# Kernel tuning notes

Hardware: AMD Instinct MI355X
Metric: run time of the kernel (lower is better)

Reference implementation:

```python
import jax, jax.numpy as jnp
import numpy as np

EMBED_DIM = 1024
NUM_HEADS = 16
HEAD_DIM = EMBED_DIM // NUM_HEADS


def setup_inputs() -> dict:
    key = jax.random.key(0)
    ks = jax.random.split(key, 9)
    B, S, D = 2, 2048, EMBED_DIM
    scale = 1.0 / np.sqrt(D)
    x = jax.random.normal(ks[0], (B, S, D), dtype=jnp.float32)
    # nn.Linear weights are stored as (out, in); y = x @ W.T + b
    Wq = jax.random.uniform(ks[1], (D, D), jnp.float32, -scale, scale)
    bq = jax.random.uniform(ks[2], (D,), jnp.float32, -scale, scale)
    Wk = jax.random.uniform(ks[3], (D, D), jnp.float32, -scale, scale)
    bk = jax.random.uniform(ks[4], (D,), jnp.float32, -scale, scale)
    Wv = jax.random.uniform(ks[5], (D, D), jnp.float32, -scale, scale)
    bv = jax.random.uniform(ks[6], (D,), jnp.float32, -scale, scale)
    Wo = jax.random.uniform(ks[7], (D, D), jnp.float32, -scale, scale)
    bo = jax.random.uniform(ks[8], (D,), jnp.float32, -scale, scale)
    return {"x": x, "Wq": Wq, "bq": bq, "Wk": Wk, "bk": bk,
            "Wv": Wv, "bv": bv, "Wo": Wo, "bo": bo}


def reference(x, Wq, bq, Wk, bk, Wv, bv, Wo, bo):
    B, S, D = x.shape
    H, Hd = NUM_HEADS, HEAD_DIM

    def split_heads(t):  # [B,S,D] -> [B,H,S,Hd]
        return t.reshape(B, S, H, Hd).transpose(0, 2, 1, 3)

    Q = split_heads(x @ Wq.T + bq)
    K = split_heads(x @ Wk.T + bk)
    V = split_heads(x @ Wv.T + bv)

    scores = jnp.einsum('bhqd,bhkd->bhqk', Q, K) / jnp.sqrt(
        jnp.asarray(Hd, dtype=x.dtype))
    attn = jax.nn.softmax(scores, axis=-1)
    out = jnp.einsum('bhqk,bhkd->bhqd', attn, V)  # [B,H,S,Hd]
    out = out.transpose(0, 2, 1, 3).reshape(B, S, D)
    return out @ Wo.T + bo
```

## Files before the change

### kernel.cpp

```cpp
#include <hip/hip_runtime.h>
#include <hip/hip_bf16.h>
#include <stdint.h>

typedef __attribute__((ext_vector_type(8))) short short8;
typedef __attribute__((ext_vector_type(4))) float f32x4;
typedef unsigned short u16;
typedef unsigned int u32;

static constexpr int S = 2048;
static constexpr int H = 16;
static constexpr int HD = 64;

__device__ __forceinline__ float fast_exp2(float x){
  return __builtin_amdgcn_exp2f(x);
}

__device__ __forceinline__ u16 f2bf(float f){
  union { float f; u32 u; } x; x.f = f;
  u32 r = x.u + 0x7fffu + ((x.u >> 16) & 1u);
  return (u16)(r >> 16);
}

__device__ __forceinline__ u32 cvt_pk_bf16(float lo, float hi){
  u32 r;
  asm("v_cvt_pk_bf16_f32 %0, %1, %2" : "=v"(r) : "v"(lo), "v"(hi));
  return r;
}

__global__ __launch_bounds__(256) void cast_all(const float* __restrict__ x,
                                                const float* __restrict__ Wq,
                                                const float* __restrict__ Wk,
                                                const float* __restrict__ Wv,
                                                const float* __restrict__ Wo,
                                                u16* __restrict__ xb,
                                                u16* __restrict__ Wb){
  int i = (blockIdx.x * 256 + threadIdx.x) * 4;
  const float* s; u16* d; int off;
  if (i < 4194304){
    s = x; d = xb; off = i;
  } else {
    int j = i - 4194304;
    int w = j >> 20;
    s = (w == 0) ? Wq : (w == 1) ? Wk : (w == 2) ? Wv : Wo;
    d = Wb + (w << 20);
    off = j & 1048575;
  }
  float4 v = *(const float4*)(s + off);
  ushort4 o;
  o.x = f2bf(v.x); o.y = f2bf(v.y); o.z = f2bf(v.z); o.w = f2bf(v.w);
  *(ushort4*)(d + off) = o;
}

__device__ __forceinline__ void gload_lds16(const void* g, void* lds_uniform){
  __builtin_amdgcn_global_load_lds(
      (const __attribute__((address_space(1))) u32*)g,
      (__attribute__((address_space(3))) u32*)lds_uniform,
      16, 0, 0);
}

__global__ __launch_bounds__(256) void gemm_qkv(const u16* __restrict__ A,
                                                const u16* __restrict__ Wall,
                                                const float* __restrict__ b0p,
                                                const float* __restrict__ b1p,
                                                const float* __restrict__ b2p,
                                                u16* __restrict__ obf){
  __shared__ __align__(16) u16 As[2*128*32];
  __shared__ __align__(16) u16 Bs[2*128*32];

  const int tid  = threadIdx.x;
  const int lane = tid & 63;
  const int wid  = tid >> 6;
  const int wm = wid >> 1, wn = wid & 1;
  const int l4 = lane >> 4, l15 = lane & 15;

  const int L = blockIdx.x + 8*blockIdx.y + 256*blockIdx.z;
  const int W = (L & 7)*96 + (L >> 3);
  const int z = W >> 8;
  const int rem = W & 255;
  const int n0 = (rem & 7) * 128;
  const int m0 = (rem >> 3) * 128;

  const u16* Bw = Wall + (size_t)z * (1024*1024);
  const float* bias = (z == 0) ? b0p : ((z == 1) ? b1p : b2p);

  f32x4 acc[4][4];
  #pragma unroll
  for (int m=0;m<4;m++)
    #pragma unroll
    for (int n=0;n<4;n++) acc[m][n] = (f32x4){0.f,0.f,0.f,0.f};

  const char* Ab = (const char*)A  + (size_t)m0 * 2048;
  const char* Bb = (const char*)Bw + (size_t)n0 * 2048;
  char* AsB = (char*)As;
  char* BsB = (char*)Bs;

  int ldsu[2], row_[2], col_[2];
  #pragma unroll
  for (int p=0;p<2;p++){
    ldsu[p] = wid*1024 + p*4096;
    int b = ldsu[p] + lane*16;
    row_[p] = b >> 6;
    col_[p] = b & 63;
  }

  #pragma unroll
  for (int p=0;p<2;p++){
    gload_lds16(Ab + (size_t)row_[p]*2048 + col_[p], AsB + ldsu[p]);
    gload_lds16(Bb + (size_t)row_[p]*2048 + col_[p], BsB + ldsu[p]);
  }
  __syncthreads();

  for (int kt = 0; kt < 32; ++kt){
    const int cur = kt & 1;
    if (kt + 1 < 32){
      const int nxt = cur ^ 1;
      const int kb = (kt + 1) * 64;
      #pragma unroll
      for (int p=0;p<2;p++){
        gload_lds16(Ab + (size_t)row_[p]*2048 + kb + col_[p], AsB + nxt*8192 + ldsu[p]);
        gload_lds16(Bb + (size_t)row_[p]*2048 + kb + col_[p], BsB + nxt*8192 + ldsu[p]);
      }
    }
    const u16* Asc = (const u16*)(AsB + cur*8192);
    const u16* Bsc = (const u16*)(BsB + cur*8192);

    short8 af[4], bfr[4];
    const int kcol = 8 * l4;
    #pragma unroll
    for (int m=0;m<4;m++)
      af[m] = *(const short8*)&Asc[(wm*64 + m*16 + l15)*32 + kcol];
    #pragma unroll
    for (int n=0;n<4;n++)
      bfr[n] = *(const short8*)&Bsc[(wn*64 + n*16 + l15)*32 + kcol];

    __builtin_amdgcn_s_setprio(1);
    #pragma unroll
    for (int m=0;m<4;m++)
      #pragma unroll
      for (int n=0;n<4;n++)
        acc[m][n] = __builtin_amdgcn_mfma_f32_16x16x32_bf16(af[m], bfr[n], acc[m][n], 0,0,0);
    __builtin_amdgcn_s_setprio(0);

    __syncthreads();
  }

  #pragma unroll
  for (int m=0;m<4;m++){
    const int rgb = m0 + wm*64 + m*16 + 4*l4;
    #pragma unroll
    for (int n=0;n<4;n++){
      const int cg = n0 + wn*64 + n*16 + l15;
      const float bb = bias[cg];
      const int bi = rgb >> 11, si = rgb & 2047;
      const int hi = cg >> 6,  hd = cg & 63;
      if (z == 2){
        u16* outz = obf + (size_t)2 * 4194304u;
        ushort4 o;
        o.x = f2bf(acc[m][n][0] + bb);
        o.y = f2bf(acc[m][n][1] + bb);
        o.z = f2bf(acc[m][n][2] + bb);
        o.w = f2bf(acc[m][n][3] + bb);
        *(ushort4*)&outz[(((size_t)(bi*16 + hi))*64 + hd)*2048 + si] = o;
      } else {
        u16* outz = obf + (size_t)z * 4194304u;
        const float sc = (z == 0) ? 0.18033688011112042f : 1.0f;
        #pragma unroll
        for (int r=0;r<4;r++)
          outz[(((size_t)(bi*16 + hi))*2048 + (si + r))*64 + hd] =
              f2bf((acc[m][n][r] + bb) * sc);
      }
    }
  }
}

__global__ __launch_bounds__(256) void gemm_out(const u16* __restrict__ A,
                                                const u16* __restrict__ Wo,
                                                const float* __restrict__ bo,
                                                float* __restrict__ ofp){
  __shared__ __align__(16) u16 As[2*64*32];
  __shared__ __align__(16) u16 Bs[2*128*32];

  const int tid  = threadIdx.x;
  const int lane = tid & 63;
  const int wid  = tid >> 6;
  const int wm = wid >> 1, wn = wid & 1;
  const int l4 = lane >> 4, l15 = lane & 15;

  const int L = blockIdx.x + 8*blockIdx.y;
  const int W = (L & 7)*64 + (L >> 3);
  const int n0 = (W & 7) * 128;
  const int m0 = (W >> 3) * 64;

  f32x4 acc[2][4];
  #pragma unroll
  for (int m=0;m<2;m++)
    #pragma unroll
    for (int n=0;n<4;n++) acc[m][n] = (f32x4){0.f,0.f,0.f,0.f};

  const char* Ab = (const char*)A  + (size_t)m0 * 2048;
  const char* Bb = (const char*)Wo + (size_t)n0 * 2048;
  char* AsB = (char*)As;
  char* BsB = (char*)Bs;

  const int ldsuA = wid*1024;
  int rowA, colA;
  { int b = ldsuA + lane*16; rowA = b >> 6; colA = b & 63; }
  int ldsuB[2], rowB[2], colB[2];
  #pragma unroll
  for (int p=0;p<2;p++){
    ldsuB[p] = wid*2048 + p*1024;
    int b = ldsuB[p] + lane*16;
    rowB[p] = b >> 6; colB[p] = b & 63;
  }

  gload_lds16(Ab + (size_t)rowA*2048 + colA, AsB + ldsuA);
  #pragma unroll
  for (int p=0;p<2;p++)
    gload_lds16(Bb + (size_t)rowB[p]*2048 + colB[p], BsB + ldsuB[p]);
  __syncthreads();

  for (int kt = 0; kt < 32; ++kt){
    const int cur = kt & 1;
    if (kt + 1 < 32){
      const int nxt = cur ^ 1;
      const int kb = (kt + 1) * 64;
      gload_lds16(Ab + (size_t)rowA*2048 + kb + colA, AsB + nxt*4096 + ldsuA);
      #pragma unroll
      for (int p=0;p<2;p++)
        gload_lds16(Bb + (size_t)rowB[p]*2048 + kb + colB[p], BsB + nxt*8192 + ldsuB[p]);
    }
    const u16* Asc = (const u16*)(AsB + cur*4096);
    const u16* Bsc = (const u16*)(BsB + cur*8192);

    short8 af[2], bfr[4];
    const int kcol = 8 * l4;
    #pragma unroll
    for (int m=0;m<2;m++)
      af[m] = *(const short8*)&Asc[(wm*32 + m*16 + l15)*32 + kcol];
    #pragma unroll
    for (int n=0;n<4;n++)
      bfr[n] = *(const short8*)&Bsc[(wn*64 + n*16 + l15)*32 + kcol];

    __builtin_amdgcn_s_setprio(1);
    #pragma unroll
    for (int m=0;m<2;m++)
      #pragma unroll
      for (int n=0;n<4;n++)
        acc[m][n] = __builtin_amdgcn_mfma_f32_16x16x32_bf16(af[m], bfr[n], acc[m][n], 0,0,0);
    __builtin_amdgcn_s_setprio(0);

    __syncthreads();
  }

  #pragma unroll
  for (int m=0;m<2;m++){
    const int rgb = m0 + wm*32 + m*16 + 4*l4;
    #pragma unroll
    for (int n=0;n<4;n++){
      const int cg = n0 + wn*64 + n*16 + l15;
      const float bb = bo[cg];
      #pragma unroll
      for (int r=0;r<4;r++)
        ofp[(size_t)(rgb + r)*1024 + cg] = acc[m][n][r] + bb;
    }
  }
}

__global__ __launch_bounds__(512, 4) void attn_fwd(const u16* __restrict__ Qg,
                                                   const u16* __restrict__ Kg,
                                                   const u16* __restrict__ Vtg,
                                                   u16* __restrict__ Og){
  __shared__ __align__(16) u16 Ks[2*2*64*64];
  __shared__ __align__(16) u16 Vs[2*2*64*64];

  const int tid  = threadIdx.x;
  const int lane = tid & 63;
  const int wid  = tid >> 6;
  const int pair = wid & 3;
  const int half = wid >> 2;
  const int l4 = lane >> 4, l15 = lane & 15;
  const int swz = l15 & 7;

  const int L = blockIdx.x + 16*blockIdx.y;
  const int W = (L & 7)*64 + (L >> 3);
  const int qb = W & 15;
  const int bh = W >> 4;
  const size_t hoff = (size_t)bh * (S * HD);

  short8 aq[2][2];
  #pragma unroll
  for (int g=0; g<2; ++g){
    const u16* qp = Qg + hoff + (size_t)(qb*128 + pair*32 + g*16 + l15) * HD;
    aq[g][0] = *(const short8*)(qp + 8*l4);
    aq[g][1] = *(const short8*)(qp + 32 + 8*l4);
  }

  const float FM = 12.0f;
  float lr[2] = {0.f, 0.f};
  f32x4 oacc[2][4];
  #pragma unroll
  for (int g=0; g<2; ++g)
    #pragma unroll
    for (int hb=0;hb<4;hb++) oacc[g][hb] = (f32x4){0.f,0.f,0.f,0.f};

  const char* Kb = (const char*)(Kg  + hoff) + (size_t)half*16*8192;
  const char* Vb = (const char*)(Vtg + hoff) + half*16*128;
  char* KsB = (char*)Ks + half*16384;
  char* VsB = (char*)Vs + half*16384;

  int ldsu[2], srcK[2], srcV[2];
  #pragma unroll
  for (int p=0;p<2;p++){
    ldsu[p] = pair*1024 + p*4096;
    int b   = ldsu[p] + lane*16;
    int row = b >> 7, cc = (b >> 4) & 7;
    int ccs = cc ^ (row & 7);
    srcK[p] = row*128  + (ccs << 4);
    srcV[p] = row*4096 + (ccs << 4);
  }

  #pragma unroll
  for (int p=0;p<2;p++){
    gload_lds16(Kb + srcK[p], KsB + ldsu[p]);
    gload_lds16(Vb + srcV[p], VsB + ldsu[p]);
  }
  __syncthreads();

  for (int kt = 0; kt < 16; ++kt){
    const int cur = kt & 1;
    if (kt + 1 < 16){
      const int nxt = cur ^ 1;
      const char* Ksrc = Kb + (size_t)(kt+1)*8192;
      const char* Vsrc = Vb + (size_t)(kt+1)*128;
      #pragma unroll
      for (int p=0;p<2;p++){
        gload_lds16(Ksrc + srcK[p], KsB + nxt*8192 + ldsu[p]);
        gload_lds16(Vsrc + srcV[p], VsB + nxt*8192 + ldsu[p]);
      }
    }

    const char* KsC = KsB + cur*8192;
    const char* VsC = VsB + cur*8192;

    f32x4 sacc[2][4];
    __builtin_amdgcn_s_setprio(1);
    #pragma unroll
    for (int nb=0;nb<4;nb++){
      const int krow = nb*16 + l15;
      short8 k0 = *(const short8*)(KsC + krow*128 + ((l4 ^ swz) << 4));
      short8 k1 = *(const short8*)(KsC + krow*128 + (((4 + l4) ^ swz) << 4));
      #pragma unroll
      for (int g=0; g<2; ++g){
        f32x4 zz = (f32x4){0.f,0.f,0.f,0.f};
        zz = __builtin_amdgcn_mfma_f32_16x16x32_bf16(k0, aq[g][0], zz, 0,0,0);
        zz = __builtin_amdgcn_mfma_f32_16x16x32_bf16(k1, aq[g][1], zz, 0,0,0);
        sacc[g][nb] = zz;
      }
    }
    __builtin_amdgcn_s_setprio(0);

    short8 apg[2][2];
    #pragma unroll
    for (int g=0; g<2; ++g){
      float rs = 0.f;
      #pragma unroll
      for (int nb=0;nb<4;nb++)
        #pragma unroll
        for (int r=0;r<4;r++){
          float p = fast_exp2(sacc[g][nb][r] - FM);
          sacc[g][nb][r] = p;
          rs += p;
        }
      lr[g] += rs;

      u32 pk[4][2];
      #pragma unroll
      for (int nb=0;nb<4;nb++){
        pk[nb][0] = cvt_pk_bf16(sacc[g][nb][0], sacc[g][nb][1]);
        pk[nb][1] = cvt_pk_bf16(sacc[g][nb][2], sacc[g][nb][3]);
      }
      #pragma unroll
      for (int ks=0; ks<2; ++ks){
        u32 a0 = pk[2*ks][0],   a1 = pk[2*ks][1];
        u32 b0 = pk[2*ks+1][0], b1 = pk[2*ks+1][1];
        asm("v_permlane32_swap_b32 %0, %1" : "+v"(a0), "+v"(b0));
        asm("v_permlane32_swap_b32 %0, %1" : "+v"(a1), "+v"(b1));
        asm("v_permlane16_swap_b32 %0, %1" : "+v"(a0), "+v"(b0));
        asm("v_permlane16_swap_b32 %0, %1" : "+v"(a1), "+v"(b1));
        union { u32 u[4]; short8 s; } cvt;
        cvt.u[0] = a0; cvt.u[1] = a1; cvt.u[2] = b0; cvt.u[3] = b1;
        apg[g][ks] = cvt.s;
      }
    }

    __builtin_amdgcn_s_setprio(1);
    #pragma unroll
    for (int ks=0;ks<2;ks++){
      #pragma unroll
      for (int hb=0;hb<4;hb++){
        const int vrow = hb*16 + l15;
        short8 bv = *(const short8*)(VsC + vrow*128 + (((ks*4 + l4) ^ swz) << 4));
        oacc[0][hb] = __builtin_amdgcn_mfma_f32_16x16x32_bf16(apg[0][ks], bv, oacc[0][hb], 0,0,0);
        oacc[1][hb] = __builtin_amdgcn_mfma_f32_16x16x32_bf16(apg[1][ks], bv, oacc[1][hb], 0,0,0);
      }
    }
    __builtin_amdgcn_s_setprio(0);
    __syncthreads();
  }

  #pragma unroll
  for (int g=0; g<2; ++g){
    lr[g] += __shfl_xor(lr[g], 16, 64);
    lr[g] += __shfl_xor(lr[g], 32, 64);
  }

  char*  scr  = (char*)Ks;
  float* lscr = (float*)Vs;
  if (half == 1){
    #pragma unroll
    for (int g=0; g<2; ++g)
      #pragma unroll
      for (int hb=0;hb<4;hb++)
        *(f32x4*)(scr + pair*8192 + (g*4+hb)*1024 + lane*16) = oacc[g][hb];
    if (lane < 16){
      lscr[pair*32 + lane]      = lr[0];
      lscr[pair*32 + 16 + lane] = lr[1];
    }
  }
  __syncthreads();

  if (half == 0){
    const int b = bh >> 4, h = bh & 15;
    #pragma unroll
    for (int g=0; g<2; ++g){
      const float lg = lr[g] + lscr[pair*32 + g*16 + l15];
      float inv[4];
      #pragma unroll
      for (int r=0;r<4;r++)
        inv[r] = 1.0f / __shfl(lg, 4*l4 + r, 64);
      #pragma unroll
      for (int hb=0;hb<4;hb++){
        f32x4 o2 = *(const f32x4*)(scr + pair*8192 + (g*4+hb)*1024 + lane*16);
        #pragma unroll
        for (int r=0;r<4;r++){
          const int si = qb*128 + pair*32 + g*16 + 4*l4 + r;
          const float v = (oacc[g][hb][r] + o2[r]) * inv[r];
          Og[(((size_t)(b*S + si))*H + h)*HD + hb*16 + l15] = f2bf(v);
        }
      }
    }
  }
}

extern "C" void kernel_launch(void* const* d_in, const int* in_sizes, int n_in,
                              void* d_out, int out_size, void* d_ws, size_t ws_size,
                              hipStream_t stream) {
  const float* x  = (const float*)d_in[0];
  const float* Wq = (const float*)d_in[1];
  const float* bq = (const float*)d_in[2];
  const float* Wk = (const float*)d_in[3];
  const float* bk = (const float*)d_in[4];
  const float* Wv = (const float*)d_in[5];
  const float* bv = (const float*)d_in[6];
  const float* Wo = (const float*)d_in[7];
  const float* bo = (const float*)d_in[8];

  char* ws = (char*)d_ws;
  u16* xb  = (u16*)(ws);
  u16* Wb  = (u16*)(ws + (size_t)8*1024*1024);
  u16* QKV = (u16*)(ws + (size_t)16*1024*1024);
  u16* AO  = (u16*)(ws + (size_t)40*1024*1024);
  float* out = (float*)d_out;

  cast_all<<<8192, 256, 0, stream>>>(x, Wq, Wk, Wv, Wo, xb, Wb);

  dim3 g1(8, 32, 3);
  gemm_qkv<<<g1, 256, 0, stream>>>(xb, Wb, bq, bk, bv, QKV);

  dim3 g2(16, 32, 1);
  attn_fwd<<<g2, 512, 0, stream>>>(QKV, QKV + 4194304, QKV + 2*4194304, AO);

  dim3 g3(8, 64, 1);
  gemm_out<<<g3, 256, 0, stream>>>(AO, Wb + 3145728, bo, out);
}
```

Measured before the change: 114.9 us.

## Triple-buffer LDS in projection GEMMs with one barrier per k-step

```diff
diff --git a/kernel.cpp b/kernel.cpp
--- a/kernel.cpp
+++ b/kernel.cpp
@@ -64,8 +64,8 @@
                                                 const float* __restrict__ b1p,
                                                 const float* __restrict__ b2p,
                                                 u16* __restrict__ obf){
-  __shared__ __align__(16) u16 As[2*128*32];
-  __shared__ __align__(16) u16 Bs[2*128*32];
+  __shared__ __align__(16) u16 As[3*128*32];
+  __shared__ __align__(16) u16 Bs[3*128*32];
 
   const int tid  = threadIdx.x;
   const int lane = tid & 63;
@@ -104,23 +104,30 @@
   }
 
   #pragma unroll
-  for (int p=0;p<2;p++){
-    gload_lds16(Ab + (size_t)row_[p]*2048 + col_[p], AsB + ldsu[p]);
-    gload_lds16(Bb + (size_t)row_[p]*2048 + col_[p], BsB + ldsu[p]);
-  }
-  __syncthreads();
-
-  for (int kt = 0; kt < 32; ++kt){
-    const int cur = kt & 1;
-    if (kt + 1 < 32){
-      const int nxt = cur ^ 1;
-      const int kb = (kt + 1) * 64;
+  for (int kt0=0; kt0<2; ++kt0){
+    const int kb = kt0 * 64;
+    #pragma unroll
+    for (int p=0;p<2;p++){
+      gload_lds16(Ab + (size_t)row_[p]*2048 + kb + col_[p], AsB + kt0*8192 + ldsu[p]);
+      gload_lds16(Bb + (size_t)row_[p]*2048 + kb + col_[p], BsB + kt0*8192 + ldsu[p]);
+    }
+  }
+
+  for (int kt = 0; kt < 31; ++kt){
+    asm volatile("s_waitcnt vmcnt(4)" ::: "memory");
+    __builtin_amdgcn_s_barrier();
+
+    if (kt + 2 < 32){
+      const int nb3 = (kt + 2) % 3;
+      const int kb = (kt + 2) * 64;
       #pragma unroll
       for (int p=0;p<2;p++){
-        gload_lds16(Ab + (size_t)row_[p]*2048 + kb + col_[p], AsB + nxt*8192 + ldsu[p]);
-        gload_lds16(Bb + (size_t)row_[p]*2048 + kb + col_[p], BsB + nxt*8192 + ldsu[p]);
-      }
-    }
+        gload_lds16(Ab + (size_t)row_[p]*2048 + kb + col_[p], AsB + nb3*8192 + ldsu[p]);
+        gload_lds16(Bb + (size_t)row_[p]*2048 + kb + col_[p], BsB + nb3*8192 + ldsu[p]);
+      }
+    }
+
+    const int cur = kt % 3;
     const u16* Asc = (const u16*)(AsB + cur*8192);
     const u16* Bsc = (const u16*)(BsB + cur*8192);
 
@@ -140,8 +147,25 @@
       for (int n=0;n<4;n++)
         acc[m][n] = __builtin_amdgcn_mfma_f32_16x16x32_bf16(af[m], bfr[n], acc[m][n], 0,0,0);
     __builtin_amdgcn_s_setprio(0);
-
-    __syncthreads();
+  }
+  {
+    asm volatile("s_waitcnt vmcnt(0)" ::: "memory");
+    __builtin_amdgcn_s_barrier();
+    const u16* Asc = (const u16*)(AsB + (31 % 3)*8192);
+    const u16* Bsc = (const u16*)(BsB + (31 % 3)*8192);
+    short8 af[4], bfr[4];
+    const int kcol = 8 * l4;
+    #pragma unroll
+    for (int m=0;m<4;m++)
+      af[m] = *(const short8*)&Asc[(wm*64 + m*16 + l15)*32 + kcol];
+    #pragma unroll
+    for (int n=0;n<4;n++)
+      bfr[n] = *(const short8*)&Bsc[(wn*64 + n*16 + l15)*32 + kcol];
+    #pragma unroll
+    for (int m=0;m<4;m++)
+      #pragma unroll
+      for (int n=0;n<4;n++)
+        acc[m][n] = __builtin_amdgcn_mfma_f32_16x16x32_bf16(af[m], bfr[n], acc[m][n], 0,0,0);
   }
 
   #pragma unroll
@@ -177,8 +201,8 @@
                                                 const u16* __restrict__ Wo,
                                                 const float* __restrict__ bo,
                                                 float* __restrict__ ofp){
-  __shared__ __align__(16) u16 As[2*64*32];
-  __shared__ __align__(16) u16 Bs[2*128*32];
+  __shared__ __align__(16) u16 As[3*64*32];
+  __shared__ __align__(16) u16 Bs[3*128*32];
 
   const int tid  = threadIdx.x;
   const int lane = tid & 63;
@@ -213,22 +237,29 @@
     rowB[p] = b >> 6; colB[p] = b & 63;
   }
 
-  gload_lds16(Ab + (size_t)rowA*2048 + colA, AsB + ldsuA);
-  #pragma unroll
-  for (int p=0;p<2;p++)
-    gload_lds16(Bb + (size_t)rowB[p]*2048 + colB[p], BsB + ldsuB[p]);
-  __syncthreads();
-
-  for (int kt = 0; kt < 32; ++kt){
-    const int cur = kt & 1;
-    if (kt + 1 < 32){
-      const int nxt = cur ^ 1;
-      const int kb = (kt + 1) * 64;
-      gload_lds16(Ab + (size_t)rowA*2048 + kb + colA, AsB + nxt*4096 + ldsuA);
+  #pragma unroll
+  for (int kt0=0; kt0<2; ++kt0){
+    const int kb = kt0 * 64;
+    gload_lds16(Ab + (size_t)rowA*2048 + kb + colA, AsB + kt0*4096 + ldsuA);
+    #pragma unroll
+    for (int p=0;p<2;p++)
+      gload_lds16(Bb + (size_t)rowB[p]*2048 + kb + colB[p], BsB + kt0*8192 + ldsuB[p]);
+  }
+
+  for (int kt = 0; kt < 31; ++kt){
+    asm volatile("s_waitcnt vmcnt(3)" ::: "memory");
+    __builtin_amdgcn_s_barrier();
+
+    if (kt + 2 < 32){
+      const int nb3 = (kt + 2) % 3;
+      const int kb = (kt + 2) * 64;
+      gload_lds16(Ab + (size_t)rowA*2048 + kb + colA, AsB + nb3*4096 + ldsuA);
       #pragma unroll
       for (int p=0;p<2;p++)
-        gload_lds16(Bb + (size_t)rowB[p]*2048 + kb + colB[p], BsB + nxt*8192 + ldsuB[p]);
-    }
+        gload_lds16(Bb + (size_t)rowB[p]*2048 + kb + colB[p], BsB + nb3*8192 + ldsuB[p]);
+    }
+
+    const int cur = kt % 3;
     const u16* Asc = (const u16*)(AsB + cur*4096);
     const u16* Bsc = (const u16*)(BsB + cur*8192);
 
@@ -248,8 +279,25 @@
       for (int n=0;n<4;n++)
         acc[m][n] = __builtin_amdgcn_mfma_f32_16x16x32_bf16(af[m], bfr[n], acc[m][n], 0,0,0);
     __builtin_amdgcn_s_setprio(0);
-
-    __syncthreads();
+  }
+  {
+    asm volatile("s_waitcnt vmcnt(0)" ::: "memory");
+    __builtin_amdgcn_s_barrier();
+    const u16* Asc = (const u16*)(AsB + (31 % 3)*4096);
+    const u16* Bsc = (const u16*)(BsB + (31 % 3)*8192);
+    short8 af[2], bfr[4];
+    const int kcol = 8 * l4;
+    #pragma unroll
+    for (int m=0;m<2;m++)
+      af[m] = *(const short8*)&Asc[(wm*32 + m*16 + l15)*32 + kcol];
+    #pragma unroll
+    for (int n=0;n<4;n++)
+      bfr[n] = *(const short8*)&Bsc[(wn*64 + n*16 + l15)*32 + kcol];
+    #pragma unroll
+    for (int m=0;m<2;m++)
+      #pragma unroll
+      for (int n=0;n<4;n++)
+        acc[m][n] = __builtin_amdgcn_mfma_f32_16x16x32_bf16(af[m], bfr[n], acc[m][n], 0,0,0);
   }
 
   #pragma unroll
```

Result: slower. 130.0 us (+13.2%).

## Load GEMM A-operand fragments directly from global into registers, bypassing LDS

Applied to the files above, without the earlier changes.

```diff
diff --git a/kernel.cpp b/kernel.cpp
--- a/kernel.cpp
+++ b/kernel.cpp
@@ -64,7 +64,6 @@
                                                 const float* __restrict__ b1p,
                                                 const float* __restrict__ b2p,
                                                 u16* __restrict__ obf){
-  __shared__ __align__(16) u16 As[2*128*32];
   __shared__ __align__(16) u16 Bs[2*128*32];
 
   const int tid  = threadIdx.x;
@@ -91,44 +90,51 @@
 
   const char* Ab = (const char*)A  + (size_t)m0 * 2048;
   const char* Bb = (const char*)Bw + (size_t)n0 * 2048;
-  char* AsB = (char*)As;
   char* BsB = (char*)Bs;
 
-  int ldsu[2], row_[2], col_[2];
+  const char* Arow[4];
+  #pragma unroll
+  for (int m=0;m<4;m++)
+    Arow[m] = Ab + (size_t)(wm*64 + m*16 + l15)*2048 + l4*16;
+
+  int ldsu[2], rowB[2], colB[2];
   #pragma unroll
   for (int p=0;p<2;p++){
     ldsu[p] = wid*1024 + p*4096;
     int b = ldsu[p] + lane*16;
-    row_[p] = b >> 6;
-    col_[p] = b & 63;
-  }
-
-  #pragma unroll
-  for (int p=0;p<2;p++){
-    gload_lds16(Ab + (size_t)row_[p]*2048 + col_[p], AsB + ldsu[p]);
-    gload_lds16(Bb + (size_t)row_[p]*2048 + col_[p], BsB + ldsu[p]);
-  }
+    rowB[p] = b >> 6;
+    colB[p] = b & 63;
+  }
+
+  #pragma unroll
+  for (int p=0;p<2;p++)
+    gload_lds16(Bb + (size_t)rowB[p]*2048 + colB[p], BsB + ldsu[p]);
+  short8 af[4];
+  #pragma unroll
+  for (int m=0;m<4;m++) af[m] = *(const short8*)(Arow[m]);
   __syncthreads();
 
+  #pragma unroll 2
   for (int kt = 0; kt < 32; ++kt){
     const int cur = kt & 1;
     if (kt + 1 < 32){
       const int nxt = cur ^ 1;
       const int kb = (kt + 1) * 64;
       #pragma unroll
-      for (int p=0;p<2;p++){
-        gload_lds16(Ab + (size_t)row_[p]*2048 + kb + col_[p], AsB + nxt*8192 + ldsu[p]);
-        gload_lds16(Bb + (size_t)row_[p]*2048 + kb + col_[p], BsB + nxt*8192 + ldsu[p]);
-      }
-    }
-    const u16* Asc = (const u16*)(AsB + cur*8192);
+      for (int p=0;p<2;p++)
+        gload_lds16(Bb + (size_t)rowB[p]*2048 + kb + colB[p], BsB + nxt*8192 + ldsu[p]);
+    }
+
+    short8 afn[4];
+    if (kt + 1 < 32){
+      const int kb = (kt + 1) * 64;
+      #pragma unroll
+      for (int m=0;m<4;m++) afn[m] = *(const short8*)(Arow[m] + kb);
+    }
+
     const u16* Bsc = (const u16*)(BsB + cur*8192);
-
-    short8 af[4], bfr[4];
+    short8 bfr[4];
     const int kcol = 8 * l4;
-    #pragma unroll
-    for (int m=0;m<4;m++)
-      af[m] = *(const short8*)&Asc[(wm*64 + m*16 + l15)*32 + kcol];
     #pragma unroll
     for (int n=0;n<4;n++)
       bfr[n] = *(const short8*)&Bsc[(wn*64 + n*16 + l15)*32 + kcol];
@@ -140,6 +146,9 @@
       for (int n=0;n<4;n++)
         acc[m][n] = __builtin_amdgcn_mfma_f32_16x16x32_bf16(af[m], bfr[n], acc[m][n], 0,0,0);
     __builtin_amdgcn_s_setprio(0);
+
+    #pragma unroll
+    for (int m=0;m<4;m++) af[m] = afn[m];
 
     __syncthreads();
   }
@@ -177,7 +186,6 @@
                                                 const u16* __restrict__ Wo,
                                                 const float* __restrict__ bo,
                                                 float* __restrict__ ofp){
-  __shared__ __align__(16) u16 As[2*64*32];
   __shared__ __align__(16) u16 Bs[2*128*32];
 
   const int tid  = threadIdx.x;
@@ -199,12 +207,13 @@
 
   const char* Ab = (const char*)A  + (size_t)m0 * 2048;
   const char* Bb = (const char*)Wo + (size_t)n0 * 2048;
-  char* AsB = (char*)As;
   char* BsB = (char*)Bs;
 
-  const int ldsuA = wid*1024;
-  int rowA, colA;
-  { int b = ldsuA + lane*16; rowA = b >> 6; colA = b & 63; }
+  const char* Arow[2];
+  #pragma unroll
+  for (int m=0;m<2;m++)
+    Arow[m] = Ab + (size_t)(wm*32 + m*16 + l15)*2048 + l4*16;
+
   int ldsuB[2], rowB[2], colB[2];
   #pragma unroll
   for (int p=0;p<2;p++){
@@ -213,30 +222,35 @@
     rowB[p] = b >> 6; colB[p] = b & 63;
   }
 
-  gload_lds16(Ab + (size_t)rowA*2048 + colA, AsB + ldsuA);
   #pragma unroll
   for (int p=0;p<2;p++)
     gload_lds16(Bb + (size_t)rowB[p]*2048 + colB[p], BsB + ldsuB[p]);
+  short8 af[2];
+  #pragma unroll
+  for (int m=0;m<2;m++) af[m] = *(const short8*)(Arow[m]);
   __syncthreads();
 
+  #pragma unroll 2
   for (int kt = 0; kt < 32; ++kt){
     const int cur = kt & 1;
     if (kt + 1 < 32){
       const int nxt = cur ^ 1;
       const int kb = (kt + 1) * 64;
-      gload_lds16(Ab + (size_t)rowA*2048 + kb + colA, AsB + nxt*4096 + ldsuA);
       #pragma unroll
       for (int p=0;p<2;p++)
         gload_lds16(Bb + (size_t)rowB[p]*2048 + kb + colB[p], BsB + nxt*8192 + ldsuB[p]);
     }
-    const u16* Asc = (const u16*)(AsB + cur*4096);
+
+    short8 afn[2];
+    if (kt + 1 < 32){
+      const int kb = (kt + 1) * 64;
+      #pragma unroll
+      for (int m=0;m<2;m++) afn[m] = *(const short8*)(Arow[m] + kb);
+    }
+
     const u16* Bsc = (const u16*)(BsB + cur*8192);
-
-    short8 af[2], bfr[4];
+    short8 bfr[4];
     const int kcol = 8 * l4;
-    #pragma unroll
-    for (int m=0;m<2;m++)
-      af[m] = *(const short8*)&Asc[(wm*32 + m*16 + l15)*32 + kcol];
     #pragma unroll
     for (int n=0;n<4;n++)
       bfr[n] = *(const short8*)&Bsc[(wn*64 + n*16 + l15)*32 + kcol];
@@ -248,6 +262,9 @@
       for (int n=0;n<4;n++)
         acc[m][n] = __builtin_amdgcn_mfma_f32_16x16x32_bf16(af[m], bfr[n], acc[m][n], 0,0,0);
     __builtin_amdgcn_s_setprio(0);
+
+    #pragma unroll
+    for (int m=0;m<2;m++) af[m] = afn[m];
 
     __syncthreads();
   }
```

Measured after the change: 146.8 us. 1.28x slower.

## Load K/V fragments directly from global memory instead of staging through LDS

Applied to the files above, without the earlier changes.

```diff
diff --git a/kernel.cpp b/kernel.cpp
--- a/kernel.cpp
+++ b/kernel.cpp
@@ -270,8 +270,8 @@
                                                    const u16* __restrict__ Kg,
                                                    const u16* __restrict__ Vtg,
                                                    u16* __restrict__ Og){
-  __shared__ __align__(16) u16 Ks[2*2*64*64];
-  __shared__ __align__(16) u16 Vs[2*2*64*64];
+  __shared__ __align__(16) char scr[4*8192];
+  __shared__ float lscr[128];
 
   const int tid  = threadIdx.x;
   const int lane = tid & 63;
@@ -279,7 +279,6 @@
   const int pair = wid & 3;
   const int half = wid >> 2;
   const int l4 = lane >> 4, l15 = lane & 15;
-  const int swz = l15 & 7;
 
   const int L = blockIdx.x + 16*blockIdx.y;
   const int W = (L & 7)*64 + (L >> 3);
@@ -303,61 +302,42 @@
     #pragma unroll
     for (int hb=0;hb<4;hb++) oacc[g][hb] = (f32x4){0.f,0.f,0.f,0.f};
 
-  const char* Kb = (const char*)(Kg  + hoff) + (size_t)half*16*8192;
-  const char* Vb = (const char*)(Vtg + hoff) + half*16*128;
-  char* KsB = (char*)Ks + half*16384;
-  char* VsB = (char*)Vs + half*16384;
-
-  int ldsu[2], srcK[2], srcV[2];
-  #pragma unroll
-  for (int p=0;p<2;p++){
-    ldsu[p] = pair*1024 + p*4096;
-    int b   = ldsu[p] + lane*16;
-    int row = b >> 7, cc = (b >> 4) & 7;
-    int ccs = cc ^ (row & 7);
-    srcK[p] = row*128  + (ccs << 4);
-    srcV[p] = row*4096 + (ccs << 4);
-  }
-
-  #pragma unroll
-  for (int p=0;p<2;p++){
-    gload_lds16(Kb + srcK[p], KsB + ldsu[p]);
-    gload_lds16(Vb + srcV[p], VsB + ldsu[p]);
-  }
-  __syncthreads();
+  const char* Kfrag = (const char*)(Kg + hoff) + (size_t)half*131072
+                      + (size_t)l15*128 + l4*16;
+  const char* Vfrag = (const char*)(Vtg + hoff) + half*2048
+                      + (size_t)l15*4096 + l4*16;
 
   for (int kt = 0; kt < 16; ++kt){
-    const int cur = kt & 1;
-    if (kt + 1 < 16){
-      const int nxt = cur ^ 1;
-      const char* Ksrc = Kb + (size_t)(kt+1)*8192;
-      const char* Vsrc = Vb + (size_t)(kt+1)*128;
-      #pragma unroll
-      for (int p=0;p<2;p++){
-        gload_lds16(Ksrc + srcK[p], KsB + nxt*8192 + ldsu[p]);
-        gload_lds16(Vsrc + srcV[p], VsB + nxt*8192 + ldsu[p]);
-      }
-    }
-
-    const char* KsC = KsB + cur*8192;
-    const char* VsC = VsB + cur*8192;
+    const char* Kt = Kfrag + (size_t)kt*8192;
+    const char* Vt = Vfrag + (size_t)kt*128;
+
+    short8 k0[4], k1[4];
+    #pragma unroll
+    for (int nb=0;nb<4;nb++){
+      k0[nb] = *(const short8*)(Kt + nb*2048);
+      k1[nb] = *(const short8*)(Kt + nb*2048 + 64);
+    }
 
     f32x4 sacc[2][4];
     __builtin_amdgcn_s_setprio(1);
     #pragma unroll
     for (int nb=0;nb<4;nb++){
-      const int krow = nb*16 + l15;
-      short8 k0 = *(const short8*)(KsC + krow*128 + ((l4 ^ swz) << 4));
-      short8 k1 = *(const short8*)(KsC + krow*128 + (((4 + l4) ^ swz) << 4));
       #pragma unroll
       for (int g=0; g<2; ++g){
         f32x4 zz = (f32x4){0.f,0.f,0.f,0.f};
-        zz = __builtin_amdgcn_mfma_f32_16x16x32_bf16(k0, aq[g][0], zz, 0,0,0);
-        zz = __builtin_amdgcn_mfma_f32_16x16x32_bf16(k1, aq[g][1], zz, 0,0,0);
+        zz = __builtin_amdgcn_mfma_f32_16x16x32_bf16(k0[nb], aq[g][0], zz, 0,0,0);
+        zz = __builtin_amdgcn_mfma_f32_16x16x32_bf16(k1[nb], aq[g][1], zz, 0,0,0);
         sacc[g][nb] = zz;
       }
     }
     __builtin_amdgcn_s_setprio(0);
+
+    short8 bv[2][4];
+    #pragma unroll
+    for (int ks=0;ks<2;ks++)
+      #pragma unroll
+      for (int hb=0;hb<4;hb++)
+        bv[ks][hb] = *(const short8*)(Vt + hb*65536 + ks*64);
 
     short8 apg[2][2];
     #pragma unroll
@@ -398,14 +378,11 @@
     for (int ks=0;ks<2;ks++){
       #pragma unroll
       for (int hb=0;hb<4;hb++){
-        const int vrow = hb*16 + l15;
-        short8 bv = *(const short8*)(VsC + vrow*128 + (((ks*4 + l4) ^ swz) << 4));
-        oacc[0][hb] = __builtin_amdgcn_mfma_f32_16x16x32_bf16(apg[0][ks], bv, oacc[0][hb], 0,0,0);
-        oacc[1][hb] = __builtin_amdgcn_mfma_f32_16x16x32_bf16(apg[1][ks], bv, oacc[1][hb], 0,0,0);
+        oacc[0][hb] = __builtin_amdgcn_mfma_f32_16x16x32_bf16(apg[0][ks], bv[ks][hb], oacc[0][hb], 0,0,0);
+        oacc[1][hb] = __builtin_amdgcn_mfma_f32_16x16x32_bf16(apg[1][ks], bv[ks][hb], oacc[1][hb], 0,0,0);
       }
     }
     __builtin_amdgcn_s_setprio(0);
-    __syncthreads();
   }
 
   #pragma unroll
@@ -414,8 +391,6 @@
     lr[g] += __shfl_xor(lr[g], 32, 64);
   }
 
-  char*  scr  = (char*)Ks;
-  float* lscr = (float*)Vs;
   if (half == 1){
     #pragma unroll
     for (int g=0; g<2; ++g)
```

Result: slower. 227.8 us (+98.3%).
